# Optimization experiments

Hardware: AMD Instinct MI355X
Metric: run time of the kernel (lower is better)

Reference implementation:

```python
import jax, jax.numpy as jnp
import numpy as np

D = 1024
B, S = 4, 2048


def setup_inputs() -> dict:
    key = jax.random.key(0)
    ks = jax.random.split(key, 6)
    sc = 1.0 / np.sqrt(D)  # truncated-normal-ish fan-in scale like hk.Linear default
    return {
        "x": jax.random.normal(ks[0], (B, S, D), dtype=jnp.float32),
        "W_amp1": jax.random.normal(ks[1], (D, D), dtype=jnp.float32) * sc,
        "b_amp1": jnp.zeros((D,), dtype=jnp.float32),
        "W_amp2": jax.random.normal(ks[2], (D, D), dtype=jnp.float32) * sc,
        "b_amp2": jnp.zeros((D,), dtype=jnp.float32),
        "vqc_params": jax.random.uniform(ks[3], (D, 4), dtype=jnp.float32, minval=-np.pi, maxval=np.pi),
        "W_post1": jax.random.normal(ks[4], (D, D), dtype=jnp.float32) * sc,
        "b_post1": jnp.zeros((D,), dtype=jnp.float32),
        "W_post2": jax.random.normal(ks[5], (D, D), dtype=jnp.float32) * sc,
        "b_post2": jnp.zeros((D,), dtype=jnp.float32),
    }


def reference(x, W_amp1, b_amp1, W_amp2, b_amp2, vqc_params,
              W_post1, b_post1, W_post2, b_post2):
    # amplitude encoder: Linear -> tanh -> Linear
    amp = jnp.tanh(x @ W_amp1 + b_amp1) @ W_amp2 + b_amp2  # [B,S,D]

    # variational quantum circuit, vectorized over channels:
    # per-channel i: out_i = amp_i*cos(theta_i/2) + Re(amp_i*sin(theta_i/2)*e^{i phi_i})
    #              = amp_i * (cos(theta_i/2) + sin(theta_i/2)*cos(phi_i))
    theta = vqc_params[:, 0]  # [D]
    phi = vqc_params[:, 1]    # [D]
    scale = jnp.cos(theta * 0.5) + jnp.sin(theta * 0.5) * jnp.cos(phi)  # [D]
    q = amp * scale  # broadcast over [B,S,D]

    # classical post: Linear -> silu -> Linear
    out = jax.nn.silu(q @ W_post1 + b_post1) @ W_post2 + b_post2
    return out
```

## Files before the change

### kernel.cpp

```cpp
#include <hip/hip_runtime.h>
#include <hip/hip_bf16.h>
#include <math.h>

#define DD 1024
#define MM 8192

typedef __attribute__((ext_vector_type(8))) short short8;
typedef __attribute__((ext_vector_type(4))) float f32x4;

__device__ inline unsigned short f32_to_bf16(float f) {
  union { float f; unsigned u; } v; v.f = f;
  unsigned u = v.u;
  u += 0x7FFFu + ((u >> 16) & 1u);
  return (unsigned short)(u >> 16);
}

__global__ void k_prep(const float* __restrict__ x, unsigned short* __restrict__ xb,
                       const float* __restrict__ w0, const float* __restrict__ w1,
                       const float* __restrict__ w2, const float* __restrict__ w3,
                       unsigned short* __restrict__ o0, unsigned short* __restrict__ o1,
                       unsigned short* __restrict__ o2, unsigned short* __restrict__ o3,
                       const float* __restrict__ vqc, float* __restrict__ sc) {
  const int bid = blockIdx.x, tid = threadIdx.x;
  if (bid < 4096) {
    const float4* xv = (const float4*)x;
    ushort4* ov = (ushort4*)xb;
    int i = bid * 256 + tid;
    #pragma unroll
    for (int r = 0; r < 2; r++, i += 4096 * 256) {
      float4 v = xv[i];
      ushort4 u;
      u.x = f32_to_bf16(v.x); u.y = f32_to_bf16(v.y);
      u.z = f32_to_bf16(v.z); u.w = f32_to_bf16(v.w);
      ov[i] = u;
    }
  } else if (bid < 8192) {
    const int rel = bid - 4096;
    const float* src; unsigned short* dst;
    switch (rel >> 10) {
      case 0: src = w0; dst = o0; break;
      case 1: src = w1; dst = o1; break;
      case 2: src = w2; dst = o2; break;
      default: src = w3; dst = o3; break;
    }
    const int t = rel & 1023;
    const int r0 = (t >> 5) * 32, c0 = (t & 31) * 32;
    __shared__ float tl[32][33];
    const int tx = tid & 31, ty = tid >> 5;
    #pragma unroll
    for (int i = 0; i < 4; i++)
      tl[ty + 8 * i][tx] = src[(size_t)(r0 + ty + 8 * i) * DD + c0 + tx];
    __syncthreads();
    #pragma unroll
    for (int i = 0; i < 4; i++)
      dst[(size_t)(c0 + ty + 8 * i) * DD + r0 + tx] = f32_to_bf16(tl[tx][ty + 8 * i]);
  } else {
    #pragma unroll
    for (int k = 0; k < 4; k++) {
      int d = tid + k * 256;
      float th = vqc[d * 4 + 0] * 0.5f, ph = vqc[d * 4 + 1];
      sc[d] = cosf(th) + sinf(th) * cosf(ph);
    }
  }
}

template <int EPI>
__launch_bounds__(256, 4)
__global__ void k_gemm(const unsigned short* __restrict__ A,
                       const unsigned short* __restrict__ Bt,
                       const float* __restrict__ bias,
                       const float* __restrict__ scale,
                       void* __restrict__ Cout) {
  constexpr int K = DD, N = DD;
  __shared__ unsigned short As[128 * 64];
  __shared__ unsigned short Bs[64 * 64];
  const int tid = threadIdx.x;
  const int wave = tid >> 6, lane = tid & 63;
  const int wr = wave >> 1, wc = wave & 1;

  const int L = blockIdx.y * gridDim.x + blockIdx.x;
  const int bx = (L >> 3) & 15;
  const int by = (L & 7) | ((L >> 7) << 3);
  const int rowA0 = by * 128, colB0 = bx * 64;

  const int lr = lane & 15, lk = (lane >> 4) * 8;
  const int srow = lane >> 3;
  const int sswz = ((lane & 7) ^ srow) * 8;

  f32x4 acc[4][2] = {};

  for (int k0 = 0; k0 < K; k0 += 64) {
    #pragma unroll
    for (int i = 0; i < 4; i++) {
      int r = i * 32 + wave * 8;
      const unsigned short* ga = A + (size_t)(rowA0 + r + srow) * K + k0 + sswz;
      __builtin_amdgcn_global_load_lds(
          (const __attribute__((address_space(1))) unsigned int*)ga,
          (__attribute__((address_space(3))) unsigned int*)(As + r * 64), 16, 0, 0);
    }
    #pragma unroll
    for (int j = 0; j < 2; j++) {
      int r = j * 32 + wave * 8;
      const unsigned short* gb = Bt + (size_t)(colB0 + r + srow) * K + k0 + sswz;
      __builtin_amdgcn_global_load_lds(
          (const __attribute__((address_space(1))) unsigned int*)gb,
          (__attribute__((address_space(3))) unsigned int*)(Bs + r * 64), 16, 0, 0);
    }
    __syncthreads();

    #pragma unroll
    for (int kk = 0; kk < 64; kk += 32) {
      short8 a[4], b[2];
      #pragma unroll
      for (int m = 0; m < 4; m++) {
        int row = wr * 64 + m * 16 + lr;
        a[m] = *(const short8*)(As + row * 64 + ((((kk + lk) >> 3) ^ (row & 7)) << 3));
      }
      #pragma unroll
      for (int n = 0; n < 2; n++) {
        int row = wc * 32 + n * 16 + lr;
        b[n] = *(const short8*)(Bs + row * 64 + ((((kk + lk) >> 3) ^ (row & 7)) << 3));
      }
      #pragma unroll
      for (int m = 0; m < 4; m++)
        #pragma unroll
        for (int n = 0; n < 2; n++)
          acc[m][n] = __builtin_amdgcn_mfma_f32_16x16x32_bf16(a[m], b[n], acc[m][n], 0, 0, 0);
    }
    __syncthreads();
  }

  const int row0 = rowA0 + wr * 64;
  const int col0 = colB0 + wc * 32;
  #pragma unroll
  for (int n = 0; n < 2; n++) {
    const int col = col0 + n * 16 + lr;
    const float bv = bias[col];
    const float sv = (EPI == 1) ? scale[col] : 0.f;
    #pragma unroll
    for (int m = 0; m < 4; m++) {
      #pragma unroll
      for (int j = 0; j < 4; j++) {
        int row = row0 + m * 16 + (lane >> 4) * 4 + j;
        float z = acc[m][n][j] + bv;
        if constexpr (EPI == 0) {
          ((unsigned short*)Cout)[(size_t)row * N + col] = f32_to_bf16(tanhf(z));
        } else if constexpr (EPI == 1) {
          ((unsigned short*)Cout)[(size_t)row * N + col] = f32_to_bf16(z * sv);
        } else if constexpr (EPI == 2) {
          ((unsigned short*)Cout)[(size_t)row * N + col] = f32_to_bf16(z / (1.f + __expf(-z)));
        } else {
          ((float*)Cout)[(size_t)row * N + col] = z;
        }
      }
    }
  }
}

extern "C" void kernel_launch(void* const* d_in, const int* in_sizes, int n_in,
                              void* d_out, int out_size, void* d_ws, size_t ws_size,
                              hipStream_t stream) {
  const float* x   = (const float*)d_in[0];
  const float* W1  = (const float*)d_in[1];
  const float* b1  = (const float*)d_in[2];
  const float* W2  = (const float*)d_in[3];
  const float* b2  = (const float*)d_in[4];
  const float* vqc = (const float*)d_in[5];
  const float* Wp1 = (const float*)d_in[6];
  const float* bp1 = (const float*)d_in[7];
  const float* Wp2 = (const float*)d_in[8];
  const float* bp2 = (const float*)d_in[9];

  char* ws = (char*)d_ws;
  unsigned short* actA = (unsigned short*)ws;
  unsigned short* actB = (unsigned short*)(ws + (16u << 20));
  unsigned short* Wt0  = (unsigned short*)(ws + (32u << 20));
  unsigned short* Wt1  = (unsigned short*)(ws + (34u << 20));
  unsigned short* Wt2  = (unsigned short*)(ws + (36u << 20));
  unsigned short* Wt3  = (unsigned short*)(ws + (38u << 20));
  float* scale = (float*)(ws + (40u << 20));

  k_prep<<<8193, 256, 0, stream>>>(x, actA, W1, W2, Wp1, Wp2,
                                   Wt0, Wt1, Wt2, Wt3, vqc, scale);

  dim3 g(DD / 64, MM / 128), b(256);
  k_gemm<0><<<g, b, 0, stream>>>(actA, Wt0, b1,  nullptr, actB);
  k_gemm<1><<<g, b, 0, stream>>>(actB, Wt1, b2,  scale,   actA);
  k_gemm<2><<<g, b, 0, stream>>>(actA, Wt2, bp1, nullptr, actB);
  k_gemm<3><<<g, b, 0, stream>>>(actB, Wt3, bp2, nullptr, d_out);
}
```

Baseline: 120.0 us.

## Double-buffer LDS tiles in GEMM to overlap global loads with MFMA

Splits the shared-memory A/B tiles into two buffers and issues the next K-tile's global-to-LDS loads before computing on the current one. A manual vmcnt wait plus barrier replaces the full syncthreads, so the loads of one tile can overlap the MFMAs of the previous one. LDS use doubles to 48KB per block, so launch bounds drop to 3 blocks per CU, which may reduce occupancy-based latency hiding.

```diff
diff --git a/kernel.cpp b/kernel.cpp
--- a/kernel.cpp
+++ b/kernel.cpp
@@ -65,15 +65,16 @@
 }
 
 template <int EPI>
-__launch_bounds__(256, 4)
+__launch_bounds__(256, 3)
 __global__ void k_gemm(const unsigned short* __restrict__ A,
                        const unsigned short* __restrict__ Bt,
                        const float* __restrict__ bias,
                        const float* __restrict__ scale,
                        void* __restrict__ Cout) {
   constexpr int K = DD, N = DD;
-  __shared__ unsigned short As[128 * 64];
-  __shared__ unsigned short Bs[64 * 64];
+  constexpr int NT = K / 64;
+  __shared__ unsigned short As[2][128 * 64];
+  __shared__ unsigned short Bs[2][64 * 64];
   const int tid = threadIdx.x;
   const int wave = tid >> 6, lane = tid & 63;
   const int wr = wave >> 1, wc = wave & 1;
@@ -87,26 +88,42 @@
   const int srow = lane >> 3;
   const int sswz = ((lane & 7) ^ srow) * 8;
 
+  const unsigned short* gA[4];
+  const unsigned short* gB[2];
+  #pragma unroll
+  for (int i = 0; i < 4; i++)
+    gA[i] = A + (size_t)(rowA0 + i * 32 + wave * 8 + srow) * K + sswz;
+  #pragma unroll
+  for (int j = 0; j < 2; j++)
+    gB[j] = Bt + (size_t)(colB0 + j * 32 + wave * 8 + srow) * K + sswz;
+
+  auto STAGE = [&](int buf, int t) {
+    const int ko = t * 64;
+    #pragma unroll
+    for (int i = 0; i < 4; i++)
+      __builtin_amdgcn_global_load_lds(
+          (const __attribute__((address_space(1))) unsigned int*)(gA[i] + ko),
+          (__attribute__((address_space(3))) unsigned int*)(&As[buf][(i * 32 + wave * 8) * 64]),
+          16, 0, 0);
+    #pragma unroll
+    for (int j = 0; j < 2; j++)
+      __builtin_amdgcn_global_load_lds(
+          (const __attribute__((address_space(1))) unsigned int*)(gB[j] + ko),
+          (__attribute__((address_space(3))) unsigned int*)(&Bs[buf][(j * 32 + wave * 8) * 64]),
+          16, 0, 0);
+  };
+
   f32x4 acc[4][2] = {};
 
-  for (int k0 = 0; k0 < K; k0 += 64) {
-    #pragma unroll
-    for (int i = 0; i < 4; i++) {
-      int r = i * 32 + wave * 8;
-      const unsigned short* ga = A + (size_t)(rowA0 + r + srow) * K + k0 + sswz;
-      __builtin_amdgcn_global_load_lds(
-          (const __attribute__((address_space(1))) unsigned int*)ga,
-          (__attribute__((address_space(3))) unsigned int*)(As + r * 64), 16, 0, 0);
-    }
-    #pragma unroll
-    for (int j = 0; j < 2; j++) {
-      int r = j * 32 + wave * 8;
-      const unsigned short* gb = Bt + (size_t)(colB0 + r + srow) * K + k0 + sswz;
-      __builtin_amdgcn_global_load_lds(
-          (const __attribute__((address_space(1))) unsigned int*)gb,
-          (__attribute__((address_space(3))) unsigned int*)(Bs + r * 64), 16, 0, 0);
-    }
-    __syncthreads();
+  STAGE(0, 0);
+  for (int t = 0; t < NT; ++t) {
+    const int cur = t & 1;
+    if (t + 1 < NT) {
+      STAGE(cur ^ 1, t + 1);
+      asm volatile("s_waitcnt vmcnt(6)\ns_barrier" ::: "memory");
+    } else {
+      asm volatile("s_waitcnt vmcnt(0)\ns_barrier" ::: "memory");
+    }
 
     #pragma unroll
     for (int kk = 0; kk < 64; kk += 32) {
@@ -114,12 +131,12 @@
       #pragma unroll
       for (int m = 0; m < 4; m++) {
         int row = wr * 64 + m * 16 + lr;
-        a[m] = *(const short8*)(As + row * 64 + ((((kk + lk) >> 3) ^ (row & 7)) << 3));
+        a[m] = *(const short8*)(&As[cur][row * 64 + ((((kk + lk) >> 3) ^ (row & 7)) << 3)]);
       }
       #pragma unroll
       for (int n = 0; n < 2; n++) {
         int row = wc * 32 + n * 16 + lr;
-        b[n] = *(const short8*)(Bs + row * 64 + ((((kk + lk) >> 3) ^ (row & 7)) << 3));
+        b[n] = *(const short8*)(&Bs[cur][row * 64 + ((((kk + lk) >> 3) ^ (row & 7)) << 3)]);
       }
       #pragma unroll
       for (int m = 0; m < 4; m++)
@@ -127,7 +144,7 @@
         for (int n = 0; n < 2; n++)
           acc[m][n] = __builtin_amdgcn_mfma_f32_16x16x32_bf16(a[m], b[n], acc[m][n], 0, 0, 0);
     }
-    __syncthreads();
+    __builtin_amdgcn_s_barrier();
   }
 
   const int row0 = rowA0 + wr * 64;
```

New measurement: 134.3 us. +11.9%, slower.

## Widen GEMM tile to 128x128 and load B fragments directly from global

Applied to the files above, without the earlier changes.

Doubles the GEMM output tile width to 128 columns per block, so each wave computes a 64x64 sub-tile with a 4x4 accumulator array. B operand fragments are now read straight from global memory into registers rather than staged through LDS, leaving only A in shared memory. The grid becomes a 1D launch of 512 blocks with a simple row-major mapping, and launch bounds drop to 2 blocks per CU. This raises data reuse per tile and removes the B LDS traffic. In exchange it adds register pressure and occupancy loss, gives uncoalesced, latency-exposed global loads for B, and drops the previous L2-friendly block swizzle.

```diff
diff --git a/kernel.cpp b/kernel.cpp
--- a/kernel.cpp
+++ b/kernel.cpp
@@ -65,7 +65,7 @@
 }
 
 template <int EPI>
-__launch_bounds__(256, 4)
+__launch_bounds__(256, 2)
 __global__ void k_gemm(const unsigned short* __restrict__ A,
                        const unsigned short* __restrict__ Bt,
                        const float* __restrict__ bias,
@@ -73,67 +73,68 @@
                        void* __restrict__ Cout) {
   constexpr int K = DD, N = DD;
   __shared__ unsigned short As[128 * 64];
-  __shared__ unsigned short Bs[64 * 64];
   const int tid = threadIdx.x;
   const int wave = tid >> 6, lane = tid & 63;
   const int wr = wave >> 1, wc = wave & 1;
 
-  const int L = blockIdx.y * gridDim.x + blockIdx.x;
-  const int bx = (L >> 3) & 15;
-  const int by = (L & 7) | ((L >> 7) << 3);
-  const int rowA0 = by * 128, colB0 = bx * 64;
+  const int L = blockIdx.x;
+  const int bx = L >> 6, by = L & 63;
+  const int rowA0 = by * 128, colB0 = bx * 128;
 
-  const int lr = lane & 15, lk = (lane >> 4) * 8;
+  const int lr = lane & 15, lks = lane >> 4;
   const int srow = lane >> 3;
   const int sswz = ((lane & 7) ^ srow) * 8;
 
-  f32x4 acc[4][2] = {};
+  const unsigned short* gA[4];
+  #pragma unroll
+  for (int i = 0; i < 4; i++)
+    gA[i] = A + (size_t)(rowA0 + i * 32 + wave * 8 + srow) * K + sswz;
+
+  const unsigned short* gBf[4];
+  #pragma unroll
+  for (int n = 0; n < 4; n++)
+    gBf[n] = Bt + (size_t)(colB0 + wc * 64 + n * 16 + lr) * K + lks * 8;
+
+  f32x4 acc[4][4] = {};
 
   for (int k0 = 0; k0 < K; k0 += 64) {
+    short8 bfr[2][4];
     #pragma unroll
-    for (int i = 0; i < 4; i++) {
-      int r = i * 32 + wave * 8;
-      const unsigned short* ga = A + (size_t)(rowA0 + r + srow) * K + k0 + sswz;
+    for (int kk2 = 0; kk2 < 2; kk2++)
+      #pragma unroll
+      for (int n = 0; n < 4; n++)
+        bfr[kk2][n] = *(const short8*)(gBf[n] + k0 + kk2 * 32);
+
+    #pragma unroll
+    for (int i = 0; i < 4; i++)
       __builtin_amdgcn_global_load_lds(
-          (const __attribute__((address_space(1))) unsigned int*)ga,
-          (__attribute__((address_space(3))) unsigned int*)(As + r * 64), 16, 0, 0);
-    }
-    #pragma unroll
-    for (int j = 0; j < 2; j++) {
-      int r = j * 32 + wave * 8;
-      const unsigned short* gb = Bt + (size_t)(colB0 + r + srow) * K + k0 + sswz;
-      __builtin_amdgcn_global_load_lds(
-          (const __attribute__((address_space(1))) unsigned int*)gb,
-          (__attribute__((address_space(3))) unsigned int*)(Bs + r * 64), 16, 0, 0);
-    }
+          (const __attribute__((address_space(1))) unsigned int*)(gA[i] + k0),
+          (__attribute__((address_space(3))) unsigned int*)(As + (i * 32 + wave * 8) * 64),
+          16, 0, 0);
+
     __syncthreads();
 
     #pragma unroll
-    for (int kk = 0; kk < 64; kk += 32) {
-      short8 a[4], b[2];
+    for (int kk2 = 0; kk2 < 2; kk2++) {
+      short8 a[4];
       #pragma unroll
       for (int m = 0; m < 4; m++) {
         int row = wr * 64 + m * 16 + lr;
-        a[m] = *(const short8*)(As + row * 64 + ((((kk + lk) >> 3) ^ (row & 7)) << 3));
-      }
-      #pragma unroll
-      for (int n = 0; n < 2; n++) {
-        int row = wc * 32 + n * 16 + lr;
-        b[n] = *(const short8*)(Bs + row * 64 + ((((kk + lk) >> 3) ^ (row & 7)) << 3));
+        a[m] = *(const short8*)(As + row * 64 + ((((kk2 * 4) + lks) ^ (row & 7)) << 3));
       }
       #pragma unroll
       for (int m = 0; m < 4; m++)
         #pragma unroll
-        for (int n = 0; n < 2; n++)
-          acc[m][n] = __builtin_amdgcn_mfma_f32_16x16x32_bf16(a[m], b[n], acc[m][n], 0, 0, 0);
+        for (int n = 0; n < 4; n++)
+          acc[m][n] = __builtin_amdgcn_mfma_f32_16x16x32_bf16(a[m], bfr[kk2][n], acc[m][n], 0, 0, 0);
     }
     __syncthreads();
   }
 
   const int row0 = rowA0 + wr * 64;
-  const int col0 = colB0 + wc * 32;
+  const int col0 = colB0 + wc * 64;
   #pragma unroll
-  for (int n = 0; n < 2; n++) {
+  for (int n = 0; n < 4; n++) {
     const int col = col0 + n * 16 + lr;
     const float bv = bias[col];
     const float sv = (EPI == 1) ? scale[col] : 0.f;
@@ -141,7 +142,7 @@
     for (int m = 0; m < 4; m++) {
       #pragma unroll
       for (int j = 0; j < 4; j++) {
-        int row = row0 + m * 16 + (lane >> 4) * 4 + j;
+        int row = row0 + m * 16 + lks * 4 + j;
         float z = acc[m][n][j] + bv;
         if constexpr (EPI == 0) {
           ((unsigned short*)Cout)[(size_t)row * N + col] = f32_to_bf16(tanhf(z));
@@ -183,7 +184,7 @@
   k_prep<<<8193, 256, 0, stream>>>(x, actA, W1, W2, Wp1, Wp2,
                                    Wt0, Wt1, Wt2, Wt3, vqc, scale);
 
-  dim3 g(DD / 64, MM / 128), b(256);
+  dim3 g(512), b(256);
   k_gemm<0><<<g, b, 0, stream>>>(actA, Wt0, b1,  nullptr, actB);
   k_gemm<1><<<g, b, 0, stream>>>(actB, Wt1, b2,  scale,   actA);
   k_gemm<2><<<g, b, 0, stream>>>(actA, Wt2, bp1, nullptr, actB);
```

Result: slower. 184.2 us (+53.6%).
